# Performance work log

Hardware: AMD Instinct MI355X
Metric: run time of the kernel (lower is better)

## Reference

```python
import jax, jax.numpy as jnp
import numpy as np

N_WIRES = 10
N_BLOCKS = 4
DIM = 2 ** N_WIRES


def _tables(n):
    # Basis-state bit tables. Wire 0 is the most-significant bit (torchquantum convention).
    s = np.arange(2 ** n)
    bits = (s[None, :] >> (n - 1 - np.arange(n))[:, None]) & 1  # [n, 2^n]
    zval = (1 - 2 * bits).astype(np.float32)  # PauliZ eigenvalue per wire per basis state
    # Composition of the circular CNOT ring (0,1),(1,2),...,(n-2,n-1),(n-1,0)
    # as a single basis permutation: state'[s] = state[P[s]].
    pairs = [(i, i + 1) for i in range(n - 1)] + [(n - 1, 0)]
    P = s.copy()
    for c, t in pairs:
        bit = (s >> (n - 1 - c)) & 1
        g = s ^ (bit << (n - 1 - t))  # CNOT maps new[s] = old[g(s)]
        P = P[g]
    return zval, P


_ZVAL_NP, _PERM_NP = _tables(N_WIRES)


def setup_inputs() -> dict:
    key = jax.random.key(0)
    k1, k2 = jax.random.split(key)
    x = jax.random.normal(k1, (2048, N_WIRES), jnp.float32)
    params = jax.random.normal(k2, (N_BLOCKS, 6, N_WIRES), jnp.float32)
    return {"x": x, "params": params}


def _rz_all(state, theta, zval):
    # RZ(theta_w) on every wire fused into one diagonal phase over the full statevector.
    # RZ = diag(e^{-i t/2}, e^{+i t/2}); exponent sign = -zval (bit0 -> -1).
    phase = jnp.exp((-0.5j) * (theta @ zval).astype(jnp.complex64))  # [2^n]
    return state * phase[None, :]


def _ry_all(state, theta, bsz):
    # RY(theta_w) on each wire w: 2x2 rotation applied along that wire's axis.
    for w in range(N_WIRES):
        left = 2 ** w
        right = DIM // (2 * left)
        s4 = state.reshape(bsz, left, 2, right)
        c = jnp.cos(theta[w] * 0.5)
        s_ = jnp.sin(theta[w] * 0.5)
        U = jnp.stack([jnp.stack([c, -s_]), jnp.stack([s_, c])]).astype(jnp.complex64)
        s4 = jnp.einsum('bixk,jx->bijk', s4, U)
        state = s4.reshape(bsz, DIM)
    return state


def reference(x, params):
    zval = jnp.asarray(_ZVAL_NP)
    perm = jnp.asarray(_PERM_NP)
    bsz = x.shape[0]
    state = jnp.zeros((bsz, DIM), jnp.complex64).at[:, 0].set(1.0)  # |0...0>
    for k in range(N_BLOCKS):
        p = params[k]
        # NOTE: the original module's "rx" layers are constructed with tq.RZ,
        # so each block is RZ, RY, RZ, CNOT-ring, RZ, RY, RZ, CNOT-ring.
        state = _rz_all(state, p[0], zval)
        state = _ry_all(state, p[1], bsz)
        state = _rz_all(state, p[2], zval)
        state = state[:, perm]
        state = _rz_all(state, p[3], zval)
        state = _ry_all(state, p[4], bsz)
        state = _rz_all(state, p[5], zval)
        state = state[:, perm]
        if k != N_BLOCKS - 1:
            # data re-uploading encoder: RZ(x[:, w]) on wire w, batch-dependent diagonal
            enc = jnp.exp((-0.5j) * (x @ zval).astype(jnp.complex64))  # [B, 2^n]
            state = state * enc
    probs = state.real ** 2 + state.imag ** 2  # [B, 2^n]
    out = probs @ zval.T  # MeasureAll PauliZ -> [B, n_wires]
    return out[None]  # [1, B, n_wires]
```

## Files before the change

kernel.cpp:

```cpp
#include <hip/hip_runtime.h>

#define NW 10

typedef float v2f __attribute__((ext_vector_type(2)));
typedef float v4f __attribute__((ext_vector_type(4)));

template<int CTRL>
__device__ __forceinline__ float fdpp(float v) {
    return __int_as_float(__builtin_amdgcn_mov_dpp(__float_as_int(v), CTRL, 0xF, 0xF, true));
}
template<int PAT>
__device__ __forceinline__ float fswz(float v) {
    return __int_as_float(__builtin_amdgcn_ds_swizzle(__float_as_int(v), PAT));
}

__device__ __forceinline__ int phi(int e) {
    return e ^ ((e & 0x10) >> 1) ^ ((e & 0x20) >> 4);
}

__global__ void precompute_kernel(const float* __restrict__ params, float4* __restrict__ tab4) {
    const int d = blockIdx.x;
    const int j = threadIdx.x;
    if (d < 7) {
        const int W = j >> 8, lane = j & 63, r = (j >> 6) & 3;
        const int s = (W << 8) | (lane << 2) | r;
        const int q = s ^ (s >> 1) ^ ((s & 1) * 0x300);
        const float* thA;
        const float* thB;
        if (d < 4) {
            thA = params + (d * 6 + 3) * NW;
            thB = params + (d * 6 + 2) * NW;
        } else {
            const int k = d - 4;
            thA = params + ((k + 1) * 6 + 0) * NW;
            thB = params + (k * 6 + 5) * NW;
        }
        float ang = 0.f;
#pragma unroll
        for (int w = 0; w < NW; ++w) {
            ang += thA[w] * (((s >> (9 - w)) & 1) ? 0.5f : -0.5f);
            ang += thB[w] * (((q >> (9 - w)) & 1) ? 0.5f : -0.5f);
        }
        float sn, cs;
        __sincosf(ang, &sn, &cs);
        tab4[d * 1024 + j] = make_float4(cs, sn, -sn, cs);
    } else if (j < 80) {
        const int ry = j / NW, w = j % NW;
        const int k = ry >> 1, i = ry & 1;
        const float* th = params + (k * 6 + (i ? 4 : 1)) * NW;
        float sn, cs;
        __sincosf(0.5f * th[w], &sn, &cs);
        float2* ryt = (float2*)(tab4 + 7 * 1024);
        ryt[j] = make_float2(cs, sn);
    }
}

__global__ __launch_bounds__(256, 4) void qsim_kernel(const float* __restrict__ x,
                                                      const v4f* __restrict__ tab4,
                                                      float* __restrict__ out) {
    __shared__ v2f buf[2][1024];
    __shared__ float sred[4][NW];

    const int t     = threadIdx.x;
    const int W     = t >> 6;
    const int lane  = t & 63;
    const int b     = blockIdx.x;
    const int ebase = lane | (W << 8);
    const float2* ry_tab = (const float2*)(tab4 + 7 * 1024);

    v2f st[4];

    const int wbase = phi(ebase);
    const int l0 = lane & 1, l1 = (lane >> 1) & 1, l2 = (lane >> 2) & 1,
              l3 = (lane >> 3) & 1, l4 = (lane >> 4) & 1, l5 = (lane >> 5) & 1;
    const int W0 = W & 1, W1 = (W >> 1) & 1;
    const int riA0 = l2 | (l4 << 1) | (l0 << 2) | (l5 << 3) | (l1 << 4) | (l3 << 5) | (W << 6);
    const int rgA  = phi(riA0);
    const int g0 = (l2 ^ l3) | ((l4 ^ l5) << 1) | ((l0 ^ l1) << 2) | ((l5 ^ W0) << 3)
                 | ((l1 ^ l2) << 4) | ((l3 ^ l4) << 5)
                 | ((W0 ^ W1) << 6) | (W1 << 7) | (l0 << 9);
    const int gP = phi(g0);

    const float* xb = x + b * NW;
    v2f xp[4];
    {
        float xv[NW];
#pragma unroll
        for (int w = 0; w < NW; ++w) xv[w] = xb[w];
        float A = 0.f;
#pragma unroll
        for (int w = 0; w < NW; ++w) A += xv[w];
        float hi = -0.5f * A;
        if (W & 2) hi += xv[0];
        if (W & 1) hi += xv[1];
#pragma unroll
        for (int j = 0; j < 6; ++j)
            hi += ((lane >> j) & 1) ? xv[7 - j] : 0.f;
        float lo[4];
        lo[0] = 0.f;   lo[1] = xv[9];
        lo[2] = xv[8]; lo[3] = xv[8] + xv[9];
#pragma unroll
        for (int r = 0; r < 4; ++r) {
            float sn, cs;
            __sincosf(hi + lo[r], &sn, &cs);
            xp[r] = (v2f){cs, sn};
        }
    }

    int bs = 0;
    v4f tq[4];

    auto pre = [&](int d) {
        const v4f* tb = tab4 + (d << 10) + ebase;
#pragma unroll
        for (int r = 0; r < 4; ++r) tq[r] = tb[r << 6];
    };
    auto apply_t = [&]() {
#pragma unroll
        for (int r = 0; r < 4; ++r)
            st[r] = st[r].x * tq[r].xy + st[r].y * tq[r].zw;
    };
    auto apply_tx = [&]() {
#pragma unroll
        for (int r = 0; r < 4; ++r) {
            const v2f c = xp[r].x * tq[r].xy + xp[r].y * tq[r].zw;
            const v2f cq = (v2f){-c.y, c.x};
            st[r] = st[r].x * c + st[r].y * cq;
        }
    };

    auto init_L1 = [&]() {
        const float2* rt = ry_tab;
        float hi = (l0 ? rt[5].y : rt[5].x);
        hi *= (l1 ? rt[3].y : rt[3].x);
        hi *= (l2 ? rt[7].y : rt[7].x);
        hi *= (l3 ? rt[2].y : rt[2].x);
        hi *= (l4 ? rt[6].y : rt[6].x);
        hi *= (l5 ? rt[4].y : rt[4].x);
        hi *= (W0 ? rt[9].y : rt[9].x);
        hi *= (W1 ? rt[8].y : rt[8].x);
        const float c1 = rt[1].x, s1 = rt[1].y, c0 = rt[0].x, s0_ = rt[0].y;
        st[0] = (v2f){hi * c1 * c0, 0.f};
        st[1] = (v2f){hi * s1 * c0, 0.f};
        st[2] = (v2f){hi * c1 * s0_, 0.f};
        st[3] = (v2f){hi * s1 * s0_, 0.f};
    };

    auto bfly_local = [&](float2 cw, int m) {
#pragma unroll
        for (int r = 0; r < 4; ++r) {
            if (!(r & m)) {
                const int r2 = r | m;
                const v2f a = st[r];
                st[r]  = cw.x * a - cw.y * st[r2];
                st[r2] = cw.y * a + cw.x * st[r2];
            }
        }
    };

    auto ry = [&](int ridx) {
        const float2* rt = ry_tab + ridx * NW;
        bfly_local(rt[9], 1);
        bfly_local(rt[8], 2);
        {   const float2 cw = rt[7]; const float ss = (lane & 1) ? cw.y : -cw.y;
#pragma unroll
            for (int r = 0; r < 4; ++r) {
                v2f p; p.x = fdpp<0xB1>(st[r].x); p.y = fdpp<0xB1>(st[r].y);
                st[r] = cw.x * st[r] + ss * p;
            }
        }
        {   const float2 cw = rt[6]; const float ss = (lane & 2) ? cw.y : -cw.y;
#pragma unroll
            for (int r = 0; r < 4; ++r) {
                v2f p; p.x = fdpp<0x4E>(st[r].x); p.y = fdpp<0x4E>(st[r].y);
                st[r] = cw.x * st[r] + ss * p;
            }
        }
        {   const float2 cw = rt[4]; const float ss = (lane & 8) ? cw.y : -cw.y;
#pragma unroll
            for (int r = 0; r < 4; ++r) {
                v2f p; p.x = fdpp<0x128>(st[r].x); p.y = fdpp<0x128>(st[r].y);
                st[r] = cw.x * st[r] + ss * p;
            }
        }
        {
            v2f* B = buf[bs]; bs ^= 1;
#pragma unroll
            for (int r = 0; r < 4; ++r)
                B[wbase + (r << 6)] = st[r];
            __syncthreads();
#pragma unroll
            for (int r = 0; r < 4; ++r)
                st[r] = B[rgA + (r << 8)];
        }
        bfly_local(rt[1], 1);
        bfly_local(rt[0], 2);
        {   const float2 cw = rt[5]; const float ss = (lane & 1) ? cw.y : -cw.y;
#pragma unroll
            for (int r = 0; r < 4; ++r) {
                v2f p; p.x = fdpp<0xB1>(st[r].x); p.y = fdpp<0xB1>(st[r].y);
                st[r] = cw.x * st[r] + ss * p;
            }
        }
        {   const float2 cw = rt[3]; const float ss = (lane & 2) ? cw.y : -cw.y;
#pragma unroll
            for (int r = 0; r < 4; ++r) {
                v2f p; p.x = fdpp<0x4E>(st[r].x); p.y = fdpp<0x4E>(st[r].y);
                st[r] = cw.x * st[r] + ss * p;
            }
        }
        {   const float2 cw = rt[2]; const float ss = (lane & 8) ? cw.y : -cw.y;
#pragma unroll
            for (int r = 0; r < 4; ++r) {
                v2f p; p.x = fdpp<0x128>(st[r].x); p.y = fdpp<0x128>(st[r].y);
                st[r] = cw.x * st[r] + ss * p;
            }
        }
    };

    auto perm = [&]() {
        v2f* B = buf[bs]; bs ^= 1;
#pragma unroll
        for (int r = 0; r < 4; ++r)
            B[wbase + (r << 6)] = st[r];
        __syncthreads();
        constexpr int xc[4] = {0, 0x1C0, 0x300, 0x2C0};
#pragma unroll
        for (int r = 0; r < 4; ++r)
            st[r] = B[gP ^ xc[r]];
    };

#pragma unroll 1
    for (int k = 0; k < 4; ++k) {
        pre(k);
        if (k == 0) init_L1();
        else        ry(2 * k);
        perm();
        apply_t();
        if (k < 3) pre(4 + k);
        ry(2 * k + 1);
        if (k < 3) {
            perm();
            apply_tx();
        }
    }

    float pr[4];
#pragma unroll
    for (int r = 0; r < 4; ++r) pr[r] = st[r].x * st[r].x + st[r].y * st[r].y;
    const float D = pr[0] - pr[1] - pr[2] + pr[3];
    const float E = pr[0] - pr[1] + pr[2] - pr[3];
    const int g2 = l3;
    const int g3 = g2 ^ l1;
    const int g4 = g3 ^ l5;
    const int g5 = g4 ^ l0;
    const int g6 = g5 ^ l4;
    const int g7 = g6 ^ l2;
    const int g8 = g7 ^ W1;
    const int g9 = g8 ^ W0;

    float acc[NW];
    acc[0] = g9 ? -E : E;
    acc[1] = D;
    acc[2] = g2 ? -D : D;
    acc[3] = g3 ? -D : D;
    acc[4] = g4 ? -D : D;
    acc[5] = g5 ? -D : D;
    acc[6] = g6 ? -D : D;
    acc[7] = g7 ? -D : D;
    acc[8] = g8 ? -D : D;
    acc[9] = g9 ? -D : D;

#pragma unroll
    for (int w = 0; w < NW; ++w) {
        float a = acc[w];
        a += fdpp<0xB1>(a);
        a += fdpp<0x4E>(a);
        a += fswz<0x101F>(a);
        a += fdpp<0x128>(a);
        a += fswz<0x401F>(a);
        a += __shfl_xor(a, 32, 64);
        acc[w] = a;
    }
    if (lane == 0) {
#pragma unroll
        for (int w = 0; w < NW; ++w) sred[W][w] = acc[w];
    }
    __syncthreads();
    if (t < NW) out[b * NW + t] = sred[0][t] + sred[1][t] + sred[2][t] + sred[3][t];
}

extern "C" void kernel_launch(void* const* d_in, const int* in_sizes, int n_in,
                              void* d_out, int out_size, void* d_ws, size_t ws_size,
                              hipStream_t stream) {
    const float* x      = (const float*)d_in[0];
    const float* params = (const float*)d_in[1];
    float* out          = (float*)d_out;
    float4* tab4        = (float4*)d_ws;
    (void)in_sizes; (void)n_in; (void)out_size; (void)ws_size;
    precompute_kernel<<<8, 1024, 0, stream>>>(params, tab4);
    qsim_kernel<<<2048, 256, 0, stream>>>(x, (const v4f*)tab4, out);
}
```

Measured before the change: 78.76 us.

## Simulate one batch sample per wavefront with 16 amplitudes per lane

Changes the mapping from one 256-thread block per sample to one wavefront per sample, so each lane holds 16 complex amplitudes. Cross-lane RY stages now use DPP, ds_swizzle and shfl, and the CNOT-ring permutation uses ds_bpermute, which removes the shared-memory round trips and __syncthreads barriers. The phase table shrinks from float4 to float2, and the final reduction writes directly without a cross-wave reduction. In exchange, register use rises (launch bounds lowered to 2) and more cross-lane permute instructions are issued, which may lower occupancy.

Result: slower. 81.08 us (+2.9%).

```diff
diff --git a/kernel.cpp b/kernel.cpp
--- a/kernel.cpp
+++ b/kernel.cpp
@@ -3,7 +3,6 @@
 #define NW 10
 
 typedef float v2f __attribute__((ext_vector_type(2)));
-typedef float v4f __attribute__((ext_vector_type(4)));
 
 template<int CTRL>
 __device__ __forceinline__ float fdpp(float v) {
@@ -13,16 +12,15 @@
 __device__ __forceinline__ float fswz(float v) {
     return __int_as_float(__builtin_amdgcn_ds_swizzle(__float_as_int(v), PAT));
 }
-
-__device__ __forceinline__ int phi(int e) {
-    return e ^ ((e & 0x10) >> 1) ^ ((e & 0x20) >> 4);
-}
-
-__global__ void precompute_kernel(const float* __restrict__ params, float4* __restrict__ tab4) {
-    const int d = blockIdx.x;
-    const int j = threadIdx.x;
-    if (d < 7) {
-        const int W = j >> 8, lane = j & 63, r = (j >> 6) & 3;
+__device__ __forceinline__ float fbperm(int addr, float v) {
+    return __int_as_float(__builtin_amdgcn_ds_bpermute(addr, __float_as_int(v)));
+}
+
+__global__ void precompute_kernel(const float* __restrict__ params, float2* __restrict__ tab) {
+    const int j = blockIdx.x * 256 + threadIdx.x;
+    if (j < 7 * 1024) {
+        const int d = j >> 10, jj = j & 1023;
+        const int W = jj >> 8, lane = jj & 63, r = (jj >> 6) & 3;
         const int s = (W << 8) | (lane << 2) | r;
         const int q = s ^ (s >> 1) ^ ((s & 1) * 0x300);
         const float* thA;
@@ -43,233 +41,219 @@
         }
         float sn, cs;
         __sincosf(ang, &sn, &cs);
-        tab4[d * 1024 + j] = make_float4(cs, sn, -sn, cs);
-    } else if (j < 80) {
-        const int ry = j / NW, w = j % NW;
-        const int k = ry >> 1, i = ry & 1;
-        const float* th = params + (k * 6 + (i ? 4 : 1)) * NW;
+        tab[j] = make_float2(cs, sn);
+    } else if (j < 7 * 1024 + 80) {
+        const int i = j - 7 * 1024;
+        const int ry = i / NW, w = i % NW;
+        const int k = ry >> 1, ii = ry & 1;
+        const float* th = params + (k * 6 + (ii ? 4 : 1)) * NW;
         float sn, cs;
         __sincosf(0.5f * th[w], &sn, &cs);
-        float2* ryt = (float2*)(tab4 + 7 * 1024);
-        ryt[j] = make_float2(cs, sn);
-    }
-}
-
-__global__ __launch_bounds__(256, 4) void qsim_kernel(const float* __restrict__ x,
-                                                      const v4f* __restrict__ tab4,
+        tab[7 * 1024 + i] = make_float2(cs, sn);
+    }
+}
+
+
+#define DPP_STAGE(CTRL, CW, BIT) do {                                          \
+    const float2 cw_ = (CW);                                                   \
+    const float ss_ = (lane & (BIT)) ? cw_.y : -cw_.y;                         \
+    _Pragma("unroll")                                                          \
+    for (int u_ = 0; u_ < 16; ++u_) {                                          \
+        v2f p_;                                                                \
+        p_.x = fdpp<CTRL>(st[u_].x);                                           \
+        p_.y = fdpp<CTRL>(st[u_].y);                                           \
+        st[u_] = cw_.x * st[u_] + ss_ * p_;                                    \
+    }                                                                          \
+} while (0)
+
+#define SWZ_STAGE(PAT, CW, BIT) do {                                           \
+    const float2 cw_ = (CW);                                                   \
+    const float ss_ = (lane & (BIT)) ? cw_.y : -cw_.y;                         \
+    v2f p_[16];                                                                \
+    _Pragma("unroll")                                                          \
+    for (int u_ = 0; u_ < 16; ++u_) {                                          \
+        p_[u_].x = fswz<PAT>(st[u_].x);                                        \
+        p_[u_].y = fswz<PAT>(st[u_].y);                                        \
+    }                                                                          \
+    _Pragma("unroll")                                                          \
+    for (int u_ = 0; u_ < 16; ++u_) st[u_] = cw_.x * st[u_] + ss_ * p_[u_];    \
+} while (0)
+
+#define X32_STAGE(CW) do {                                                     \
+    const float2 cw_ = (CW);                                                   \
+    const float ss_ = (lane & 32) ? cw_.y : -cw_.y;                            \
+    v2f p_[16];                                                                \
+    _Pragma("unroll")                                                          \
+    for (int u_ = 0; u_ < 16; ++u_) {                                          \
+        p_[u_].x = __shfl_xor(st[u_].x, 32, 64);                               \
+        p_[u_].y = __shfl_xor(st[u_].y, 32, 64);                               \
+    }                                                                          \
+    _Pragma("unroll")                                                          \
+    for (int u_ = 0; u_ < 16; ++u_) st[u_] = cw_.x * st[u_] + ss_ * p_[u_];    \
+} while (0)
+
+__global__ __launch_bounds__(256, 2) void qsim_kernel(const float* __restrict__ x,
+                                                      const float2* __restrict__ tab,
                                                       float* __restrict__ out) {
-    __shared__ v2f buf[2][1024];
-    __shared__ float sred[4][NW];
-
-    const int t     = threadIdx.x;
-    const int W     = t >> 6;
-    const int lane  = t & 63;
-    const int b     = blockIdx.x;
-    const int ebase = lane | (W << 8);
-    const float2* ry_tab = (const float2*)(tab4 + 7 * 1024);
-
-    v2f st[4];
-
-    const int wbase = phi(ebase);
+    const int t    = threadIdx.x;
+    const int W    = t >> 6;
+    const int lane = t & 63;
+    const int b    = blockIdx.x * 4 + W;
+    const float2* ry_tab = tab + 7 * 1024;
+
     const int l0 = lane & 1, l1 = (lane >> 1) & 1, l2 = (lane >> 2) & 1,
               l3 = (lane >> 3) & 1, l4 = (lane >> 4) & 1, l5 = (lane >> 5) & 1;
-    const int W0 = W & 1, W1 = (W >> 1) & 1;
-    const int riA0 = l2 | (l4 << 1) | (l0 << 2) | (l5 << 3) | (l1 << 4) | (l3 << 5) | (W << 6);
-    const int rgA  = phi(riA0);
-    const int g0 = (l2 ^ l3) | ((l4 ^ l5) << 1) | ((l0 ^ l1) << 2) | ((l5 ^ W0) << 3)
-                 | ((l1 ^ l2) << 4) | ((l3 ^ l4) << 5)
-                 | ((W0 ^ W1) << 6) | (W1 << 7) | (l0 << 9);
-    const int gP = phi(g0);
-
-    const float* xb = x + b * NW;
-    v2f xp[4];
+
+    const int lp = (l0 ^ l1) | ((l1 ^ l2) << 1) | ((l2 ^ l3) << 2)
+                 | ((l3 ^ l4) << 3) | ((l4 ^ l5) << 4) | (l5 << 5);
+    const int pa0 = lp << 2;
+    const int pa1 = pa0 ^ 128;
+    const int par = l0 ^ l1 ^ l2 ^ l3 ^ l4 ^ l5;
+
+    v2f st[16];
+    float2 xp[16];
+    float2 tq[16];
+
     {
+        const float* xb = x + b * NW;
         float xv[NW];
 #pragma unroll
         for (int w = 0; w < NW; ++w) xv[w] = xb[w];
         float A = 0.f;
 #pragma unroll
         for (int w = 0; w < NW; ++w) A += xv[w];
-        float hi = -0.5f * A;
-        if (W & 2) hi += xv[0];
-        if (W & 1) hi += xv[1];
-#pragma unroll
-        for (int j = 0; j < 6; ++j)
-            hi += ((lane >> j) & 1) ? xv[7 - j] : 0.f;
-        float lo[4];
-        lo[0] = 0.f;   lo[1] = xv[9];
-        lo[2] = xv[8]; lo[3] = xv[8] + xv[9];
-#pragma unroll
-        for (int r = 0; r < 4; ++r) {
+        float hb = -0.5f * A;
+        if (l0) hb += xv[7];
+        if (l1) hb += xv[6];
+        if (l2) hb += xv[5];
+        if (l3) hb += xv[4];
+        if (l4) hb += xv[3];
+        if (l5) hb += xv[2];
+#pragma unroll
+        for (int u = 0; u < 16; ++u) {
+            float ang = hb;
+            if (u & 1) ang += xv[9];
+            if (u & 2) ang += xv[8];
+            if (u & 4) ang += xv[1];
+            if (u & 8) ang += xv[0];
             float sn, cs;
-            __sincosf(hi + lo[r], &sn, &cs);
-            xp[r] = (v2f){cs, sn};
-        }
-    }
-
-    int bs = 0;
-    v4f tq[4];
+            __sincosf(ang, &sn, &cs);
+            xp[u] = make_float2(cs, sn);
+        }
+    }
 
     auto pre = [&](int d) {
-        const v4f* tb = tab4 + (d << 10) + ebase;
-#pragma unroll
-        for (int r = 0; r < 4; ++r) tq[r] = tb[r << 6];
-    };
-    auto apply_t = [&]() {
-#pragma unroll
-        for (int r = 0; r < 4; ++r)
-            st[r] = st[r].x * tq[r].xy + st[r].y * tq[r].zw;
-    };
-    auto apply_tx = [&]() {
-#pragma unroll
-        for (int r = 0; r < 4; ++r) {
-            const v2f c = xp[r].x * tq[r].xy + xp[r].y * tq[r].zw;
-            const v2f cq = (v2f){-c.y, c.x};
-            st[r] = st[r].x * c + st[r].y * cq;
-        }
-    };
-
-    auto init_L1 = [&]() {
-        const float2* rt = ry_tab;
-        float hi = (l0 ? rt[5].y : rt[5].x);
-        hi *= (l1 ? rt[3].y : rt[3].x);
-        hi *= (l2 ? rt[7].y : rt[7].x);
-        hi *= (l3 ? rt[2].y : rt[2].x);
-        hi *= (l4 ? rt[6].y : rt[6].x);
-        hi *= (l5 ? rt[4].y : rt[4].x);
-        hi *= (W0 ? rt[9].y : rt[9].x);
-        hi *= (W1 ? rt[8].y : rt[8].x);
-        const float c1 = rt[1].x, s1 = rt[1].y, c0 = rt[0].x, s0_ = rt[0].y;
-        st[0] = (v2f){hi * c1 * c0, 0.f};
-        st[1] = (v2f){hi * s1 * c0, 0.f};
-        st[2] = (v2f){hi * c1 * s0_, 0.f};
-        st[3] = (v2f){hi * s1 * s0_, 0.f};
-    };
-
-    auto bfly_local = [&](float2 cw, int m) {
-#pragma unroll
-        for (int r = 0; r < 4; ++r) {
-            if (!(r & m)) {
-                const int r2 = r | m;
-                const v2f a = st[r];
-                st[r]  = cw.x * a - cw.y * st[r2];
-                st[r2] = cw.y * a + cw.x * st[r2];
+        const float2* tb = tab + (d << 10) + lane;
+#pragma unroll
+        for (int u = 0; u < 16; ++u)
+            tq[u] = tb[((u & 3) << 6) | ((u >> 2) << 8)];
+    };
+
+    auto initC = [&]() {
+        const float2 r9 = ry_tab[9], r8 = ry_tab[8], r7 = ry_tab[7], r6 = ry_tab[6],
+                     r5 = ry_tab[5], r4 = ry_tab[4], r3 = ry_tab[3], r2 = ry_tab[2],
+                     r1 = ry_tab[1], r0 = ry_tab[0];
+        float P6 = (l0 ? r7.y : r7.x) * (l1 ? r6.y : r6.x) * (l2 ? r5.y : r5.x)
+                 * (l3 ? r4.y : r4.x) * (l4 ? r3.y : r3.x) * (l5 ? r2.y : r2.x);
+#pragma unroll
+        for (int u = 0; u < 16; ++u) {
+            float v = P6 * ((u & 1) ? r9.y : r9.x) * ((u & 2) ? r8.y : r8.x)
+                         * ((u & 4) ? r1.y : r1.x) * ((u & 8) ? r0.y : r0.x);
+            st[u] = (v2f){v, 0.f};
+        }
+    };
+
+    auto bflyL = [&](float2 cw, int m) {
+#pragma unroll
+        for (int u = 0; u < 16; ++u)
+            if (!(u & m)) {
+                const int v = u | m;
+                const v2f a = st[u];
+                st[u] = cw.x * a - cw.y * st[v];
+                st[v] = cw.y * a + cw.x * st[v];
             }
-        }
     };
 
     auto ry = [&](int ridx) {
         const float2* rt = ry_tab + ridx * NW;
-        bfly_local(rt[9], 1);
-        bfly_local(rt[8], 2);
-        {   const float2 cw = rt[7]; const float ss = (lane & 1) ? cw.y : -cw.y;
-#pragma unroll
-            for (int r = 0; r < 4; ++r) {
-                v2f p; p.x = fdpp<0xB1>(st[r].x); p.y = fdpp<0xB1>(st[r].y);
-                st[r] = cw.x * st[r] + ss * p;
+        bflyL(rt[9], 1);
+        bflyL(rt[8], 2);
+        bflyL(rt[1], 4);
+        bflyL(rt[0], 8);
+        DPP_STAGE(0xB1, rt[7], 1);
+        DPP_STAGE(0x4E, rt[6], 2);
+        SWZ_STAGE(0x101F, rt[5], 4);
+        DPP_STAGE(0x128, rt[4], 8);
+        SWZ_STAGE(0x401F, rt[3], 16);
+        X32_STAGE(rt[2]);
+    };
+
+    auto permApply = [&](int mode) {
+        v2f ns[16];
+#pragma unroll
+        for (int u = 0; u < 16; ++u) {
+            const int u0 = u & 1, u1 = (u >> 1) & 1, u2 = (u >> 2) & 1, u3 = (u >> 3) & 1;
+            const int a = (u0 ^ u1) | (u1 << 1) | ((u0 ^ u2 ^ u3) << 2) | ((u0 ^ u3) << 3);
+            const v2f v = (par ^ u2) ? st[a ^ 2] : st[a];
+            const int ad = u2 ? pa1 : pa0;
+            ns[u].x = fbperm(ad, v.x);
+            ns[u].y = fbperm(ad, v.y);
+        }
+#pragma unroll
+        for (int u = 0; u < 16; ++u) {
+            float cx = tq[u].x, cy = tq[u].y;
+            if (mode) {
+                const float tx = cx, ty = cy;
+                cx = tx * xp[u].x - ty * xp[u].y;
+                cy = tx * xp[u].y + ty * xp[u].x;
             }
-        }
-        {   const float2 cw = rt[6]; const float ss = (lane & 2) ? cw.y : -cw.y;
-#pragma unroll
-            for (int r = 0; r < 4; ++r) {
-                v2f p; p.x = fdpp<0x4E>(st[r].x); p.y = fdpp<0x4E>(st[r].y);
-                st[r] = cw.x * st[r] + ss * p;
-            }
-        }
-        {   const float2 cw = rt[4]; const float ss = (lane & 8) ? cw.y : -cw.y;
-#pragma unroll
-            for (int r = 0; r < 4; ++r) {
-                v2f p; p.x = fdpp<0x128>(st[r].x); p.y = fdpp<0x128>(st[r].y);
-                st[r] = cw.x * st[r] + ss * p;
-            }
-        }
-        {
-            v2f* B = buf[bs]; bs ^= 1;
-#pragma unroll
-            for (int r = 0; r < 4; ++r)
-                B[wbase + (r << 6)] = st[r];
-            __syncthreads();
-#pragma unroll
-            for (int r = 0; r < 4; ++r)
-                st[r] = B[rgA + (r << 8)];
-        }
-        bfly_local(rt[1], 1);
-        bfly_local(rt[0], 2);
-        {   const float2 cw = rt[5]; const float ss = (lane & 1) ? cw.y : -cw.y;
-#pragma unroll
-            for (int r = 0; r < 4; ++r) {
-                v2f p; p.x = fdpp<0xB1>(st[r].x); p.y = fdpp<0xB1>(st[r].y);
-                st[r] = cw.x * st[r] + ss * p;
-            }
-        }
-        {   const float2 cw = rt[3]; const float ss = (lane & 2) ? cw.y : -cw.y;
-#pragma unroll
-            for (int r = 0; r < 4; ++r) {
-                v2f p; p.x = fdpp<0x4E>(st[r].x); p.y = fdpp<0x4E>(st[r].y);
-                st[r] = cw.x * st[r] + ss * p;
-            }
-        }
-        {   const float2 cw = rt[2]; const float ss = (lane & 8) ? cw.y : -cw.y;
-#pragma unroll
-            for (int r = 0; r < 4; ++r) {
-                v2f p; p.x = fdpp<0x128>(st[r].x); p.y = fdpp<0x128>(st[r].y);
-                st[r] = cw.x * st[r] + ss * p;
-            }
-        }
-    };
-
-    auto perm = [&]() {
-        v2f* B = buf[bs]; bs ^= 1;
-#pragma unroll
-        for (int r = 0; r < 4; ++r)
-            B[wbase + (r << 6)] = st[r];
-        __syncthreads();
-        constexpr int xc[4] = {0, 0x1C0, 0x300, 0x2C0};
-#pragma unroll
-        for (int r = 0; r < 4; ++r)
-            st[r] = B[gP ^ xc[r]];
+            st[u] = (v2f){cx * ns[u].x - cy * ns[u].y,
+                          cy * ns[u].x + cx * ns[u].y};
+        }
     };
 
 #pragma unroll 1
     for (int k = 0; k < 4; ++k) {
         pre(k);
-        if (k == 0) init_L1();
+        if (k == 0) initC();
         else        ry(2 * k);
-        perm();
-        apply_t();
+        permApply(0);
         if (k < 3) pre(4 + k);
         ry(2 * k + 1);
-        if (k < 3) {
-            perm();
-            apply_tx();
-        }
-    }
-
-    float pr[4];
-#pragma unroll
-    for (int r = 0; r < 4; ++r) pr[r] = st[r].x * st[r].x + st[r].y * st[r].y;
-    const float D = pr[0] - pr[1] - pr[2] + pr[3];
-    const float E = pr[0] - pr[1] + pr[2] - pr[3];
-    const int g2 = l3;
-    const int g3 = g2 ^ l1;
-    const int g4 = g3 ^ l5;
-    const int g5 = g4 ^ l0;
-    const int g6 = g5 ^ l4;
-    const int g7 = g6 ^ l2;
-    const int g8 = g7 ^ W1;
-    const int g9 = g8 ^ W0;
+        if (k < 3) permApply(1);
+    }
+
+    float pr[16];
+#pragma unroll
+    for (int u = 0; u < 16; ++u) pr[u] = st[u].x * st[u].x + st[u].y * st[u].y;
+
+    float q0[4], q1[4], q2[4];
+#pragma unroll
+    for (int g = 0; g < 4; ++g) {
+        const float a = pr[4 * g] + pr[4 * g + 1], bb = pr[4 * g + 2] + pr[4 * g + 3];
+        const float c = pr[4 * g] - pr[4 * g + 1], d = pr[4 * g + 2] - pr[4 * g + 3];
+        q0[g] = a + bb;
+        q1[g] = a - bb;
+        q2[g] = c - d;
+    }
+    const float R23   = q0[0] - q0[1] - q0[2] + q0[3];
+    const float R123  = q1[0] - q1[1] - q1[2] + q1[3];
+    const float R0123 = q2[0] - q2[1] - q2[2] + q2[3];
+    const float R012  = q2[0] - q2[1] + q2[2] - q2[3];
+
+    const int P5 = l5, P4 = l4 ^ P5, P3 = l3 ^ P4, P2 = l2 ^ P3, P1 = l1 ^ P2, P0 = l0 ^ P1;
 
     float acc[NW];
-    acc[0] = g9 ? -E : E;
-    acc[1] = D;
-    acc[2] = g2 ? -D : D;
-    acc[3] = g3 ? -D : D;
-    acc[4] = g4 ? -D : D;
-    acc[5] = g5 ? -D : D;
-    acc[6] = g6 ? -D : D;
-    acc[7] = g7 ? -D : D;
-    acc[8] = g8 ? -D : D;
-    acc[9] = g9 ? -D : D;
+    acc[0] = P0 ? -R012 : R012;
+    acc[1] = R23;
+    acc[2] = P5 ? -R23 : R23;
+    acc[3] = P4 ? -R23 : R23;
+    acc[4] = P3 ? -R23 : R23;
+    acc[5] = P2 ? -R23 : R23;
+    acc[6] = P1 ? -R23 : R23;
+    acc[7] = P0 ? -R23 : R23;
+    acc[8] = P0 ? -R123 : R123;
+    acc[9] = P0 ? -R0123 : R0123;
 
 #pragma unroll
     for (int w = 0; w < NW; ++w) {
@@ -283,11 +267,13 @@
         acc[w] = a;
     }
     if (lane == 0) {
-#pragma unroll
-        for (int w = 0; w < NW; ++w) sred[W][w] = acc[w];
-    }
-    __syncthreads();
-    if (t < NW) out[b * NW + t] = sred[0][t] + sred[1][t] + sred[2][t] + sred[3][t];
+        float2* o = (float2*)(out + b * NW);
+        o[0] = make_float2(acc[0], acc[1]);
+        o[1] = make_float2(acc[2], acc[3]);
+        o[2] = make_float2(acc[4], acc[5]);
+        o[3] = make_float2(acc[6], acc[7]);
+        o[4] = make_float2(acc[8], acc[9]);
+    }
 }
 
 extern "C" void kernel_launch(void* const* d_in, const int* in_sizes, int n_in,
@@ -296,8 +282,8 @@
     const float* x      = (const float*)d_in[0];
     const float* params = (const float*)d_in[1];
     float* out          = (float*)d_out;
-    float4* tab4        = (float4*)d_ws;
+    float2* tab         = (float2*)d_ws;
     (void)in_sizes; (void)n_in; (void)out_size; (void)ws_size;
-    precompute_kernel<<<8, 1024, 0, stream>>>(params, tab4);
-    qsim_kernel<<<2048, 256, 0, stream>>>(x, (const v4f*)tab4, out);
-}
+    precompute_kernel<<<29, 256, 0, stream>>>(params, tab);
+    qsim_kernel<<<512, 256, 0, stream>>>(x, tab, out);
+}
```
